# Kernel tuning notes

Hardware: AMD Instinct MI355X
Metric: run time of the kernel (lower is better)

The kernel has to match this reference:

```python
import jax, jax.numpy as jnp
import numpy as np
import math

IN_F, OUT_F, RANK, ALPHA = 4096, 4096, 16, 32
SCALING = ALPHA / RANK


def setup_inputs() -> dict:
    key = jax.random.key(0)
    k_x, k_w, k_a = jax.random.split(key, 3)
    x = jax.random.normal(k_x, (4, 2048, IN_F), dtype=jnp.float32)
    weight = jax.random.normal(k_w, (OUT_F, IN_F), dtype=jnp.float32)
    bias = jnp.zeros((OUT_F,), dtype=jnp.float32)
    lora_A = jax.random.normal(k_a, (RANK, IN_F), dtype=jnp.float32) * math.sqrt(2.0 / RANK)
    lora_B = jnp.zeros((OUT_F, RANK), dtype=jnp.float32)
    return {"x": x, "weight": weight, "bias": bias, "lora_A": lora_A, "lora_B": lora_B}


def reference(x, weight, bias, lora_A, lora_B):
    # base: x @ W^T + b    [B,S,out]
    base = jnp.einsum("bsi,oi->bso", x, weight) + bias
    # faithful to source: materialize full rank-update matrix (B @ A) [out,in]
    delta_w = lora_B @ lora_A
    lora = jnp.einsum("bsi,oi->bso", x, delta_w) * SCALING
    return base + lora
```

## Files before the change

### kernel.cpp

```cpp
#include <hip/hip_runtime.h>
#include <hip/hip_bf16.h>

#define IN_F   4096
#define OUT_F  4096
#define M_ROWS 8192
#define RANK   16
#define SCALING 2.0f

#define BM 256
#define BN 256
#define BK 64
#define NT (IN_F / BK)

typedef __attribute__((ext_vector_type(8))) short bf16x8;
typedef __attribute__((ext_vector_type(4))) float f32x4;
typedef unsigned short ushort_t;

template<int V> struct ic { static constexpr int value = V; };

__device__ __forceinline__ short f2b(float f) {
    union { float f; unsigned u; } c; c.f = f;
    unsigned r = (c.u + 0x7FFFu + ((c.u >> 16) & 1u)) >> 16;
    return (short)r;
}

__device__ __forceinline__ float4 ld4(const float* p) { return *(const float4*)p; }

__device__ __forceinline__ float4 s4(float4 v, float s) {
    v.x *= s; v.y *= s; v.z *= s; v.w *= s; return v;
}

__device__ __forceinline__ bf16x8 pack8(float4 a, float4 b) {
    bf16x8 r;
    r[0] = f2b(a.x); r[1] = f2b(a.y); r[2] = f2b(a.z); r[3] = f2b(a.w);
    r[4] = f2b(b.x); r[5] = f2b(b.y); r[6] = f2b(b.z); r[7] = f2b(b.w);
    return r;
}

__device__ __forceinline__ void gload16(const void* g, void* l) {
    __builtin_amdgcn_global_load_lds(
        (const __attribute__((address_space(1))) unsigned int*)g,
        (__attribute__((address_space(3))) unsigned int*)l, 16, 0, 0);
}

__global__ __launch_bounds__(256) void cvt3_kernel(const float* __restrict__ x,
                                                   const float* __restrict__ w,
                                                   const float* __restrict__ a,
                                                   ushort_t* __restrict__ xb,
                                                   ushort_t* __restrict__ wb,
                                                   ushort_t* __restrict__ ab) {
    const int n8x = M_ROWS * IN_F / 8;
    const int n8w = OUT_F * IN_F / 8;
    const int n8a = RANK * IN_F / 8;
    const int ntot = n8x + n8w + n8a;
    int i = blockIdx.x * blockDim.x + threadIdx.x;
    const int stride = gridDim.x * blockDim.x;
    for (; i < ntot; i += stride) {
        const float* src; ushort_t* dst; int j;
        if (i < n8x)            { src = x; dst = xb; j = i; }
        else if (i < n8x + n8w) { src = w; dst = wb; j = i - n8x; }
        else                    { src = a; dst = ab; j = i - n8x - n8w; }
        const float* p = src + (size_t)j * 8;
        *(bf16x8*)(dst + (size_t)j * 8) = pack8(ld4(p), ld4(p + 4));
    }
}

__global__ __launch_bounds__(64) void lora_t_mfma(const ushort_t* __restrict__ xb,
                                                  const ushort_t* __restrict__ ab,
                                                  float* __restrict__ T) {
    const int lane = threadIdx.x & 63;
    const int r0 = blockIdx.x * 16;
    const int l15 = lane & 15, lk = lane >> 4;
    const ushort_t* xr = xb + (size_t)(r0 + l15) * IN_F + lk * 8;
    const ushort_t* ar = ab + (size_t)l15 * IN_F + lk * 8;
    f32x4 acc = (f32x4){0.f, 0.f, 0.f, 0.f};
    for (int k0 = 0; k0 < IN_F; k0 += 32) {
        bf16x8 af = *(const bf16x8*)(xr + k0);
        bf16x8 bf = *(const bf16x8*)(ar + k0);
        acc = __builtin_amdgcn_mfma_f32_16x16x32_bf16(af, bf, acc, 0, 0, 0);
    }
#pragma unroll
    for (int v = 0; v < 4; v++)
        T[(size_t)(r0 + lk * 4 + v) * RANK + l15] = acc[v];
}

#define FENCE() asm volatile("" ::: "memory")

__global__ __launch_bounds__(512, 1) void gemm8p(
        const ushort_t* __restrict__ xb, const ushort_t* __restrict__ wb,
        const float* __restrict__ bias, const float* __restrict__ lora_B,
        const float* __restrict__ T, float* __restrict__ out) {

    __shared__ __align__(16) ushort_t As[2][BM * BK];
    __shared__ __align__(16) ushort_t Bs[2][BN * BK];

    const int tid  = threadIdx.x;
    const int lane = tid & 63, wv = tid >> 6;
    const int wm = wv >> 2, wn = wv & 3;
    const int l15 = lane & 15, lk = lane >> 4;

    const int bid = blockIdx.x;
    const int swz = (bid & 7) * 64 + (bid >> 3);
    const int by = swz >> 4, bx = swz & 15;
    const int brow = by * BM, bcol = bx * BN;

    const int off0 = wv * 2048 + lane * 16;
    const int off1 = off0 + 1024;
    const int row0 = off0 >> 7, row1 = off1 >> 7;
    const int sc0 = ((off0 & 127) ^ ((row0 & 7) << 4)) >> 1;
    const int sc1 = ((off1 & 127) ^ ((row1 & 7) << 4)) >> 1;
    const int ldst = wv * 1024;

    const size_t gA0 = (size_t)(brow + row0) * IN_F + sc0;
    const size_t gA1 = (size_t)(brow + row1) * IN_F + sc1;
    const size_t gB0 = (size_t)(bcol + row0) * IN_F + sc0;
    const size_t gB1 = (size_t)(bcol + row1) * IN_F + sc1;

    auto SA = [&](int h, int kt, auto BB) {
        constexpr int b = decltype(BB)::value;
        const size_t ho = (size_t)h * (128 * IN_F);
        gload16(xb + gA0 + ho + kt * 64, &As[b][h * 8192 + ldst]);
        gload16(xb + gA1 + ho + kt * 64, &As[b][h * 8192 + ldst + 512]);
    };
    auto SB = [&](int h, int kt, auto BB) {
        constexpr int b = decltype(BB)::value;
        const size_t ho = (size_t)h * (128 * IN_F);
        gload16(wb + gB0 + ho + kt * 64, &Bs[b][h * 8192 + ldst]);
        gload16(wb + gB1 + ho + kt * 64, &Bs[b][h * 8192 + ldst + 512]);
    };

    const int cb0 = (lk * 16) ^ ((l15 & 7) << 4);
    const int cb1 = (64 + lk * 16) ^ ((l15 & 7) << 4);
    const int am = wm * 128, bn = wn * 64;

    f32x4 acc[8][4];
#pragma unroll
    for (int m = 0; m < 8; m++)
#pragma unroll
        for (int n = 0; n < 4; n++) acc[m][n] = (f32x4){0.f, 0.f, 0.f, 0.f};

    bf16x8 af[8], bfq[8];

    SA(0, 0, ic<0>{}); SA(1, 0, ic<0>{});
    SB(0, 0, ic<0>{}); SB(1, 0, ic<0>{});
    SB(0, 1, ic<1>{}); SA(0, 1, ic<1>{});
    asm volatile("s_waitcnt vmcnt(4)" ::: "memory");
    __builtin_amdgcn_s_barrier();
    FENCE();

    auto TB = [&](auto CC, int tt) {
        constexpr int c = decltype(CC)::value;
        constexpr int n = c ^ 1;
        const int kt1 = (tt + 1 < NT) ? tt + 1 : NT - 1;
        const int kt2 = (tt + 2 < NT) ? tt + 2 : NT - 1;

#pragma unroll
        for (int mi = 0; mi < 4; mi++) {
            const char* rp = (const char*)&As[c][0] + (am + mi * 16 + l15) * 128;
            af[mi * 2]     = *(const bf16x8*)(rp + cb0);
            af[mi * 2 + 1] = *(const bf16x8*)(rp + cb1);
        }
#pragma unroll
        for (int ni = 0; ni < 2; ni++) {
            const char* rp = (const char*)&Bs[c][0] + (bn + ni * 16 + l15) * 128;
            bfq[ni * 2]     = *(const bf16x8*)(rp + cb0);
            bfq[ni * 2 + 1] = *(const bf16x8*)(rp + cb1);
        }
        SA(1, kt1, ic<n>{});
        __builtin_amdgcn_s_setprio(1);
#pragma unroll
        for (int mi = 0; mi < 4; mi++)
#pragma unroll
            for (int ni = 0; ni < 2; ni++)
#pragma unroll
                for (int ks = 0; ks < 2; ks++)
                    acc[mi][ni] = __builtin_amdgcn_mfma_f32_16x16x32_bf16(
                        af[mi * 2 + ks], bfq[ni * 2 + ks], acc[mi][ni], 0, 0, 0);
        __builtin_amdgcn_s_setprio(0);
        FENCE();
        __builtin_amdgcn_s_barrier();
        FENCE();

#pragma unroll
        for (int ni = 0; ni < 2; ni++) {
            const char* rp = (const char*)&Bs[c][0] + (bn + 32 + ni * 16 + l15) * 128;
            bfq[(2 + ni) * 2]     = *(const bf16x8*)(rp + cb0);
            bfq[(2 + ni) * 2 + 1] = *(const bf16x8*)(rp + cb1);
        }
        SB(1, kt1, ic<n>{});
        __builtin_amdgcn_s_setprio(1);
#pragma unroll
        for (int mi = 0; mi < 4; mi++)
#pragma unroll
            for (int ni = 0; ni < 2; ni++)
#pragma unroll
                for (int ks = 0; ks < 2; ks++)
                    acc[mi][2 + ni] = __builtin_amdgcn_mfma_f32_16x16x32_bf16(
                        af[mi * 2 + ks], bfq[(2 + ni) * 2 + ks], acc[mi][2 + ni], 0, 0, 0);
        __builtin_amdgcn_s_setprio(0);
        FENCE();
        __builtin_amdgcn_s_barrier();
        FENCE();

#pragma unroll
        for (int mi = 0; mi < 4; mi++) {
            const char* rp = (const char*)&As[c][0] + (am + 64 + mi * 16 + l15) * 128;
            af[mi * 2]     = *(const bf16x8*)(rp + cb0);
            af[mi * 2 + 1] = *(const bf16x8*)(rp + cb1);
        }
        SB(0, kt2, ic<c>{});
        __builtin_amdgcn_s_setprio(1);
#pragma unroll
        for (int mi = 0; mi < 4; mi++)
#pragma unroll
            for (int ni = 0; ni < 2; ni++)
#pragma unroll
                for (int ks = 0; ks < 2; ks++)
                    acc[4 + mi][2 + ni] = __builtin_amdgcn_mfma_f32_16x16x32_bf16(
                        af[mi * 2 + ks], bfq[(2 + ni) * 2 + ks], acc[4 + mi][2 + ni], 0, 0, 0);
        __builtin_amdgcn_s_setprio(0);
        FENCE();
        __builtin_amdgcn_s_barrier();
        FENCE();

        SA(0, kt2, ic<c>{});
        __builtin_amdgcn_s_setprio(1);
#pragma unroll
        for (int mi = 0; mi < 4; mi++)
#pragma unroll
            for (int ni = 0; ni < 2; ni++)
#pragma unroll
                for (int ks = 0; ks < 2; ks++)
                    acc[4 + mi][ni] = __builtin_amdgcn_mfma_f32_16x16x32_bf16(
                        af[mi * 2 + ks], bfq[ni * 2 + ks], acc[4 + mi][ni], 0, 0, 0);
        __builtin_amdgcn_s_setprio(0);
        asm volatile("s_waitcnt vmcnt(4)" ::: "memory");
        __builtin_amdgcn_s_barrier();
        FENCE();
    };

    for (int tt = 0; tt < NT; tt += 2) {
        TB(ic<0>{}, tt);
        TB(ic<1>{}, tt + 1);
    }

    asm volatile("s_waitcnt vmcnt(0)" ::: "memory");
    __builtin_amdgcn_s_barrier();
    {
        const int r = tid >> 1, hh = tid & 1;
        ushort_t* LA = &As[0][0];
        ushort_t* LB = &Bs[0][0];
        if (hh == 0) {
            const float* tp = T + (size_t)(brow + r) * RANK;
            *(bf16x8*)&LA[r * 32]     = pack8(s4(ld4(tp), SCALING), s4(ld4(tp + 4), SCALING));
            *(bf16x8*)&LA[r * 32 + 8] = pack8(s4(ld4(tp + 8), SCALING), s4(ld4(tp + 12), SCALING));
            const float* bp = lora_B + (size_t)(bcol + r) * RANK;
            *(bf16x8*)&LB[r * 32]     = pack8(ld4(bp), ld4(bp + 4));
            *(bf16x8*)&LB[r * 32 + 8] = pack8(ld4(bp + 8), ld4(bp + 12));
        } else {
            bf16x8 z;
#pragma unroll
            for (int i = 0; i < 8; i++) z[i] = 0;
            *(bf16x8*)&LA[r * 32 + 16] = z; *(bf16x8*)&LA[r * 32 + 24] = z;
            *(bf16x8*)&LB[r * 32 + 16] = z; *(bf16x8*)&LB[r * 32 + 24] = z;
        }
    }
    __syncthreads();
    {
        const ushort_t* LA = &As[0][0];
        const ushort_t* LB = &Bs[0][0];
        bf16x8 bfL[4];
#pragma unroll
        for (int n = 0; n < 4; n++)
            bfL[n] = *(const bf16x8*)&LB[(bn + n * 16 + l15) * 32 + lk * 8];
#pragma unroll
        for (int m = 0; m < 8; m++) {
            bf16x8 afL = *(const bf16x8*)&LA[(am + m * 16 + l15) * 32 + lk * 8];
#pragma unroll
            for (int n = 0; n < 4; n++)
                acc[m][n] = __builtin_amdgcn_mfma_f32_16x16x32_bf16(afL, bfL[n], acc[m][n], 0, 0, 0);
        }
    }

#pragma unroll
    for (int n = 0; n < 4; n++) {
        const int col = bcol + bn + n * 16 + l15;
        const float bv = bias[col];
#pragma unroll
        for (int m = 0; m < 8; m++) {
            const int row0_ = brow + am + m * 16 + lk * 4;
#pragma unroll
            for (int v = 0; v < 4; v++)
                out[(size_t)(row0_ + v) * OUT_F + col] = acc[m][n][v] + bv;
        }
    }
}

__global__ __launch_bounds__(256) void lora_t_kernel(const float* __restrict__ x,
                                                     const float* __restrict__ lora_A,
                                                     float* __restrict__ T) {
    const int t   = threadIdx.x;
    const int row = blockIdx.x * 16 + (t >> 4);
    const int rr  = t & 15;
    const float* xr = x + (size_t)row * IN_F;
    const float* ar = lora_A + (size_t)rr * IN_F;
    float acc = 0.f;
#pragma unroll 8
    for (int k = 0; k < IN_F; k += 4) {
        float4 xv = ld4(xr + k);
        float4 av = ld4(ar + k);
        acc += xv.x * av.x + xv.y * av.y + xv.z * av.z + xv.w * av.w;
    }
    T[row * RANK + rr] = acc;
}

__global__ __launch_bounds__(256) void lora_gemm_kernel(
        const float* __restrict__ x, const float* __restrict__ w,
        const float* __restrict__ bias, const float* __restrict__ lora_B,
        const float* __restrict__ T, float* __restrict__ out) {

    __shared__ __align__(16) short As[128][32];
    __shared__ __align__(16) short Bs[128][32];

    const int t    = threadIdx.x;
    const int brow = blockIdx.y * 128;
    const int bcol = blockIdx.x * 128;
    const int srow  = t >> 1;
    const int shalf = (t & 1) << 4;
    const float* xa = x + (size_t)(brow + srow) * IN_F + shalf;
    const float* wb = w + (size_t)(bcol + srow) * IN_F + shalf;
    const int lane = t & 63;
    const int wv   = t >> 6;
    const int wr   = wv >> 1, wc = wv & 1;
    const int l15  = lane & 15, lk = lane >> 4;

    f32x4 acc[4][4];
#pragma unroll
    for (int m = 0; m < 4; m++)
#pragma unroll
        for (int n = 0; n < 4; n++)
            acc[m][n] = (f32x4){0.f, 0.f, 0.f, 0.f};

    for (int k0 = 0; k0 < IN_F; k0 += 32) {
        float4 a0 = ld4(xa + k0);      float4 a1 = ld4(xa + k0 + 4);
        float4 a2 = ld4(xa + k0 + 8);  float4 a3 = ld4(xa + k0 + 12);
        float4 b0 = ld4(wb + k0);      float4 b1 = ld4(wb + k0 + 4);
        float4 b2 = ld4(wb + k0 + 8);  float4 b3 = ld4(wb + k0 + 12);

        __syncthreads();
        *(bf16x8*)&As[srow][shalf]     = pack8(a0, a1);
        *(bf16x8*)&As[srow][shalf + 8] = pack8(a2, a3);
        *(bf16x8*)&Bs[srow][shalf]     = pack8(b0, b1);
        *(bf16x8*)&Bs[srow][shalf + 8] = pack8(b2, b3);
        __syncthreads();

        bf16x8 af[4], bf[4];
#pragma unroll
        for (int m = 0; m < 4; m++) af[m] = *(bf16x8*)&As[wr * 64 + m * 16 + l15][lk * 8];
#pragma unroll
        for (int n = 0; n < 4; n++) bf[n] = *(bf16x8*)&Bs[wc * 64 + n * 16 + l15][lk * 8];
#pragma unroll
        for (int m = 0; m < 4; m++)
#pragma unroll
            for (int n = 0; n < 4; n++)
                acc[m][n] = __builtin_amdgcn_mfma_f32_16x16x32_bf16(af[m], bf[n], acc[m][n], 0, 0, 0);
    }

    __syncthreads();
    if (shalf == 0) {
        const float* tp = T + (size_t)(brow + srow) * RANK;
        *(bf16x8*)&As[srow][0] = pack8(s4(ld4(tp), SCALING), s4(ld4(tp + 4), SCALING));
        *(bf16x8*)&As[srow][8] = pack8(s4(ld4(tp + 8), SCALING), s4(ld4(tp + 12), SCALING));
        const float* bp = lora_B + (size_t)(bcol + srow) * RANK;
        *(bf16x8*)&Bs[srow][0] = pack8(ld4(bp), ld4(bp + 4));
        *(bf16x8*)&Bs[srow][8] = pack8(ld4(bp + 8), ld4(bp + 12));
    } else {
        bf16x8 z;
#pragma unroll
        for (int i = 0; i < 8; i++) z[i] = 0;
        *(bf16x8*)&As[srow][16] = z; *(bf16x8*)&As[srow][24] = z;
        *(bf16x8*)&Bs[srow][16] = z; *(bf16x8*)&Bs[srow][24] = z;
    }
    __syncthreads();
    {
        bf16x8 af[4], bf[4];
#pragma unroll
        for (int m = 0; m < 4; m++) af[m] = *(bf16x8*)&As[wr * 64 + m * 16 + l15][lk * 8];
#pragma unroll
        for (int n = 0; n < 4; n++) bf[n] = *(bf16x8*)&Bs[wc * 64 + n * 16 + l15][lk * 8];
#pragma unroll
        for (int m = 0; m < 4; m++)
#pragma unroll
            for (int n = 0; n < 4; n++)
                acc[m][n] = __builtin_amdgcn_mfma_f32_16x16x32_bf16(af[m], bf[n], acc[m][n], 0, 0, 0);
    }

    const int ocol0 = bcol + wc * 64 + l15;
#pragma unroll
    for (int n = 0; n < 4; n++) {
        const int col = ocol0 + n * 16;
        const float bv = bias[col];
#pragma unroll
        for (int m = 0; m < 4; m++) {
            const int row0 = brow + wr * 64 + m * 16 + lk * 4;
#pragma unroll
            for (int v = 0; v < 4; v++) {
                out[(size_t)(row0 + v) * OUT_F + col] = acc[m][n][v] + bv;
            }
        }
    }
}

extern "C" void kernel_launch(void* const* d_in, const int* in_sizes, int n_in,
                              void* d_out, int out_size, void* d_ws, size_t ws_size,
                              hipStream_t stream) {
    const float* x      = (const float*)d_in[0];
    const float* w      = (const float*)d_in[1];
    const float* bias   = (const float*)d_in[2];
    const float* lora_A = (const float*)d_in[3];
    const float* lora_B = (const float*)d_in[4];
    float* out = (float*)d_out;

    const size_t OFF_T = 0;
    const size_t OFF_A = 524288;
    const size_t OFF_W = 655360;
    const size_t OFF_X = 34209792;
    const size_t WS_NEED = 101318656;

    if (ws_size >= WS_NEED) {
        char* ws = (char*)d_ws;
        float*    T   = (float*)(ws + OFF_T);
        ushort_t* ab  = (ushort_t*)(ws + OFF_A);
        ushort_t* wbp = (ushort_t*)(ws + OFF_W);
        ushort_t* xbp = (ushort_t*)(ws + OFF_X);

        cvt3_kernel<<<3072, 256, 0, stream>>>(x, w, lora_A, xbp, wbp, ab);
        lora_t_mfma<<<M_ROWS / 16, 64, 0, stream>>>(xbp, ab, T);
        gemm8p<<<(M_ROWS / BM) * (OUT_F / BN), 512, 0, stream>>>(xbp, wbp, bias, lora_B, T, out);
    } else {
        float* T = (float*)d_ws;
        lora_t_kernel<<<M_ROWS / 16, 256, 0, stream>>>(x, lora_A, T);
        dim3 grid(OUT_F / 128, M_ROWS / 128);
        lora_gemm_kernel<<<grid, 256, 0, stream>>>(x, w, bias, lora_B, T, out);
    }
}
```

Measured before the change: 315.5 us.

## Fuse x conversion and LoRA x·A^T projection into one prep kernel

Replaces the separate fp32→bf16 conversion kernel and the LoRA T=x·A^T kernel with one prep kernel. Some blocks convert x rows and immediately feed the converted fragments to MFMA against A, splitting K across four waves and reducing the partial sums in shared memory. The remaining blocks convert W. This removes a kernel launch and the re-read of bf16 x, and gives the T computation more parallelism, at the cost of possible load imbalance between the two block roles.

```diff
diff --git a/kernel.cpp b/kernel.cpp
--- a/kernel.cpp
+++ b/kernel.cpp
@@ -43,48 +43,53 @@
         (__attribute__((address_space(3))) unsigned int*)l, 16, 0, 0);
 }
 
-__global__ __launch_bounds__(256) void cvt3_kernel(const float* __restrict__ x,
-                                                   const float* __restrict__ w,
-                                                   const float* __restrict__ a,
-                                                   ushort_t* __restrict__ xb,
-                                                   ushort_t* __restrict__ wb,
-                                                   ushort_t* __restrict__ ab) {
-    const int n8x = M_ROWS * IN_F / 8;
-    const int n8w = OUT_F * IN_F / 8;
-    const int n8a = RANK * IN_F / 8;
-    const int ntot = n8x + n8w + n8a;
-    int i = blockIdx.x * blockDim.x + threadIdx.x;
-    const int stride = gridDim.x * blockDim.x;
-    for (; i < ntot; i += stride) {
-        const float* src; ushort_t* dst; int j;
-        if (i < n8x)            { src = x; dst = xb; j = i; }
-        else if (i < n8x + n8w) { src = w; dst = wb; j = i - n8x; }
-        else                    { src = a; dst = ab; j = i - n8x - n8w; }
-        const float* p = src + (size_t)j * 8;
-        *(bf16x8*)(dst + (size_t)j * 8) = pack8(ld4(p), ld4(p + 4));
-    }
-}
-
-__global__ __launch_bounds__(64) void lora_t_mfma(const ushort_t* __restrict__ xb,
-                                                  const ushort_t* __restrict__ ab,
-                                                  float* __restrict__ T) {
-    const int lane = threadIdx.x & 63;
-    const int r0 = blockIdx.x * 16;
-    const int l15 = lane & 15, lk = lane >> 4;
-    const ushort_t* xr = xb + (size_t)(r0 + l15) * IN_F + lk * 8;
-    const ushort_t* ar = ab + (size_t)l15 * IN_F + lk * 8;
-    f32x4 acc = (f32x4){0.f, 0.f, 0.f, 0.f};
-    for (int k0 = 0; k0 < IN_F; k0 += 32) {
-        bf16x8 af = *(const bf16x8*)(xr + k0);
-        bf16x8 bf = *(const bf16x8*)(ar + k0);
-        acc = __builtin_amdgcn_mfma_f32_16x16x32_bf16(af, bf, acc, 0, 0, 0);
-    }
-#pragma unroll
-    for (int v = 0; v < 4; v++)
-        T[(size_t)(r0 + lk * 4 + v) * RANK + l15] = acc[v];
-}
-
 #define FENCE() asm volatile("" ::: "memory")
+
+__global__ __launch_bounds__(256) void prep_kernel(
+        const float* __restrict__ x, const float* __restrict__ w,
+        const float* __restrict__ lora_A,
+        ushort_t* __restrict__ xb, ushort_t* __restrict__ wb,
+        float* __restrict__ T) {
+    const int tid = threadIdx.x;
+    if (blockIdx.x < 512) {
+        __shared__ float part[4][16][16];
+        const int lane = tid & 63, wv = tid >> 6;
+        const int l15 = lane & 15, lk = lane >> 4;
+        const int r0 = blockIdx.x * 16;
+        const int kq = wv * 1024;
+        const float*  xr = x      + (size_t)(r0 + l15) * IN_F + kq + lk * 8;
+        const float*  ar = lora_A + (size_t)l15        * IN_F + kq + lk * 8;
+        ushort_t*     xw = xb     + (size_t)(r0 + l15) * IN_F + kq + lk * 8;
+        f32x4 accT = (f32x4){0.f, 0.f, 0.f, 0.f};
+#pragma unroll 4
+        for (int it = 0; it < 1024; it += 32) {
+            bf16x8 xf = pack8(ld4(xr + it), ld4(xr + it + 4));
+            *(bf16x8*)(xw + it) = xf;
+            bf16x8 afr = pack8(ld4(ar + it), ld4(ar + it + 4));
+            accT = __builtin_amdgcn_mfma_f32_16x16x32_bf16(xf, afr, accT, 0, 0, 0);
+        }
+#pragma unroll
+        for (int v = 0; v < 4; v++) part[wv][lk * 4 + v][l15] = accT[v];
+        __syncthreads();
+        if (tid < 64) {
+#pragma unroll
+            for (int e = 0; e < 4; e++) {
+                const int idx = tid * 4 + e;
+                const int i = idx >> 4, j = idx & 15;
+                T[(size_t)(r0 + i) * RANK + j] =
+                    part[0][i][j] + part[1][i][j] + part[2][i][j] + part[3][i][j];
+            }
+        }
+    } else {
+        const int n8w = OUT_F * IN_F / 8;
+        int i = (blockIdx.x - 512) * 256 + tid;
+        const int stride = 1024 * 256;
+        for (; i < n8w; i += stride) {
+            const float* p = w + (size_t)i * 8;
+            *(bf16x8*)(wb + (size_t)i * 8) = pack8(ld4(p), ld4(p + 4));
+        }
+    }
+}
 
 __global__ __launch_bounds__(512, 1) void gemm8p(
         const ushort_t* __restrict__ xb, const ushort_t* __restrict__ wb,
@@ -426,16 +431,15 @@
     const size_t OFF_W = 655360;
     const size_t OFF_X = 34209792;
     const size_t WS_NEED = 101318656;
+    (void)OFF_A;
 
     if (ws_size >= WS_NEED) {
         char* ws = (char*)d_ws;
         float*    T   = (float*)(ws + OFF_T);
-        ushort_t* ab  = (ushort_t*)(ws + OFF_A);
         ushort_t* wbp = (ushort_t*)(ws + OFF_W);
         ushort_t* xbp = (ushort_t*)(ws + OFF_X);
 
-        cvt3_kernel<<<3072, 256, 0, stream>>>(x, w, lora_A, xbp, wbp, ab);
-        lora_t_mfma<<<M_ROWS / 16, 64, 0, stream>>>(xbp, ab, T);
+        prep_kernel<<<1536, 256, 0, stream>>>(x, w, lora_A, xbp, wbp, T);
         gemm8p<<<(M_ROWS / BM) * (OUT_F / BN), 512, 0, stream>>>(xbp, wbp, bias, lora_B, T, out);
     } else {
         float* T = (float*)d_ws;
```

New measurement: 304.4 us. 1.04x faster.
